# Optimization experiments

Measured on AMD Instinct MI355X. Metric: run time of the kernel, lower is better.

The kernel has to match this reference:

```python
import jax, jax.numpy as jnp
import numpy as np

EMB = 64
B, L = 4096, 200
N_USERS, N_ITEMS, N_RATE, N_RANK, N_SPEC = 100000, 100000, 6, 128, 64
EPS = 1e-10


def _mlp2(x, w1, b1, w2, b2):
    # Linear -> ReLU -> Linear  (torch MLP: in -> in//2 -> out)
    return jax.nn.relu(x @ w1 + b1) @ w2 + b2


def setup_inputs() -> dict:
    key = jax.random.key(0)
    ks = jax.random.split(key, 32)
    s = 0.02
    d = {}
    d["user_tab"] = jax.random.normal(ks[0], (N_USERS, EMB), jnp.float32) * s
    d["item_tab"] = jax.random.normal(ks[1], (N_ITEMS, EMB), jnp.float32) * s
    d["rating_tab"] = jax.random.normal(ks[2], (N_RATE, EMB), jnp.float32) * s
    d["ranking_tab"] = jax.random.normal(ks[3], (N_RANK, EMB), jnp.float32) * s
    d["species_tab"] = jax.random.normal(ks[4], (N_SPEC, EMB), jnp.float32) * s
    # g_u: MLP(2E -> E): Linear(2E, E), ReLU, Linear(E, E)
    d["gu_w1"] = jax.random.normal(ks[5], (2 * EMB, EMB), jnp.float32) * s
    d["gu_b1"] = jnp.zeros((EMB,), jnp.float32)
    d["gu_w2"] = jax.random.normal(ks[6], (EMB, EMB), jnp.float32) * s
    d["gu_b2"] = jnp.zeros((EMB,), jnp.float32)
    # item_users_attn: MLP(2E -> 1): Linear(2E, E), ReLU, Linear(E, 1)
    d["at_w1"] = jax.random.normal(ks[7], (2 * EMB, EMB), jnp.float32) * s
    d["at_b1"] = jnp.zeros((EMB,), jnp.float32)
    d["at_w2"] = jax.random.normal(ks[8], (EMB, 1), jnp.float32) * s
    d["at_b2"] = jnp.zeros((1,), jnp.float32)
    # aggr_users: Linear(E, E) + ReLU
    d["ag_w"] = jax.random.normal(ks[9], (EMB, EMB), jnp.float32) * s
    d["ag_b"] = jnp.zeros((EMB,), jnp.float32)
    # final mlp: Linear(2E,E) ReLU Linear(E,E) ReLU Linear(E,E) ReLU
    d["m_w1"] = jax.random.normal(ks[10], (2 * EMB, EMB), jnp.float32) * s
    d["m_b1"] = jnp.zeros((EMB,), jnp.float32)
    d["m_w2"] = jax.random.normal(ks[11], (EMB, EMB), jnp.float32) * s
    d["m_b2"] = jnp.zeros((EMB,), jnp.float32)
    d["m_w3"] = jax.random.normal(ks[12], (EMB, EMB), jnp.float32) * s
    d["m_b3"] = jnp.zeros((EMB,), jnp.float32)
    # int inputs
    d["iids"] = jax.random.randint(ks[13], (B,), 0, N_ITEMS, jnp.int64 if jax.config.jax_enable_x64 else jnp.int32)
    d["i_user_pad"] = jnp.stack([
        jax.random.randint(ks[14], (B, L), 0, N_USERS),
        jax.random.randint(ks[15], (B, L), 0, N_RATE)], axis=-1)
    d["i_userk_pad"] = jnp.stack([
        jax.random.randint(ks[16], (B, L), 0, N_USERS),
        jax.random.randint(ks[17], (B, L), 0, N_RANK)], axis=-1)
    d["i_user_species_pad"] = jnp.stack([
        jax.random.randint(ks[18], (B, L), 0, N_USERS),
        jax.random.randint(ks[19], (B, L), 0, N_SPEC)], axis=-1)
    return d


def _attn_aggregate(f_jt, q_j, mask, at_w1, at_b1, at_w2, at_b2, ag_w, ag_b):
    # masked exp-softmax attention over neighbor axis + weighted sum + aggregator
    mu = _mlp2(jnp.concatenate([f_jt, q_j], axis=-1), at_w1, at_b1, at_w2, at_b2)[..., 0]  # [B, L]
    mu = jnp.exp(mu) * mask
    mu = mu / (jnp.sum(mu, axis=1, keepdims=True) + EPS)
    z = jnp.einsum('bl,bld->bd', mu, f_jt)
    return jax.nn.relu(z @ ag_w + ag_b)


def reference(user_tab, item_tab, rating_tab, ranking_tab, species_tab,
              gu_w1, gu_b1, gu_w2, gu_b2,
              at_w1, at_b1, at_w2, at_b2,
              ag_w, ag_b,
              m_w1, m_b1, m_w2, m_b2, m_w3, m_b3,
              iids, i_user_pad, i_userk_pad, i_user_species_pad):
    p_t = user_tab[i_user_pad[:, :, 0]]            # [B, L, E]
    i_user_er = rating_tab[i_user_pad[:, :, 1]]    # [B, L, E]
    mask = (i_user_pad[:, :, 0] > 0).astype(p_t.dtype)  # [B, L]
    q_j = jnp.broadcast_to(item_tab[iids][:, None, :], p_t.shape)  # [B, L, E]

    # branch 1: species-modulated
    spec = species_tab[i_user_species_pad[:, :, 1]]
    f1 = _mlp2(jnp.concatenate([p_t, spec], axis=-1), gu_w1, gu_b1, gu_w2, gu_b2) * i_user_er
    z_j1 = _attn_aggregate(f1, q_j, mask, at_w1, at_b1, at_w2, at_b2, ag_w, ag_b)

    # branch 2: ranking-modulated, double g_u
    nk = ranking_tab[i_userk_pad[:, :, 1]]
    f2 = _mlp2(jnp.concatenate([p_t, i_user_er], axis=-1), gu_w1, gu_b1, gu_w2, gu_b2) * nk
    f2 = _mlp2(jnp.concatenate([p_t, f2], axis=-1), gu_w1, gu_b1, gu_w2, gu_b2)
    z_j2 = _attn_aggregate(f2, q_j, mask, at_w1, at_b1, at_w2, at_b2, ag_w, ag_b)

    # final 3-layer MLP with ReLU after each layer
    h = jax.nn.relu(jnp.concatenate([z_j1, z_j2], axis=1) @ m_w1 + m_b1)
    h = jax.nn.relu(h @ m_w2 + m_b2)
    h = jax.nn.relu(h @ m_w3 + m_b3)
    return h
```

## Files before the change

### kernel.cpp

```cpp
#include <hip/hip_runtime.h>

#define EPSV 1e-10f
#define XS 68

typedef __attribute__((__ext_vector_type__(8))) short  bhalf8;
typedef __attribute__((__ext_vector_type__(4))) float  f4;
typedef __attribute__((__ext_vector_type__(4))) unsigned u4;

#define MFMA(a,b,c) __builtin_amdgcn_mfma_f32_16x16x32_bf16(a,b,c,0,0,0)

__device__ __forceinline__ bhalf8 ldb16(const unsigned* p) {
    u4 v = *(const u4*)p;
    return __builtin_bit_cast(bhalf8, v);
}

__device__ __forceinline__ void split8(f4 a, f4 b, bhalf8& h, bhalf8& l) {
    float ff[8] = {a[0],a[1],a[2],a[3],b[0],b[1],b[2],b[3]};
    unsigned uh[8]; float fl[8];
#pragma unroll
    for (int i = 0; i < 8; ++i) {
        unsigned bits = __float_as_uint(ff[i]);
        uh[i] = bits & 0xFFFF0000u;
        fl[i] = ff[i] - __uint_as_float(uh[i]);
    }
    u4 hv = { (uh[0]>>16)|uh[1], (uh[2]>>16)|uh[3], (uh[4]>>16)|uh[5], (uh[6]>>16)|uh[7] };
    u4 lv = { (__float_as_uint(fl[0])>>16)|(__float_as_uint(fl[1])&0xFFFF0000u),
              (__float_as_uint(fl[2])>>16)|(__float_as_uint(fl[3])&0xFFFF0000u),
              (__float_as_uint(fl[4])>>16)|(__float_as_uint(fl[5])&0xFFFF0000u),
              (__float_as_uint(fl[6])>>16)|(__float_as_uint(fl[7])&0xFFFF0000u) };
    h = __builtin_bit_cast(bhalf8, hv);
    l = __builtin_bit_cast(bhalf8, lv);
}

__device__ __forceinline__ void gemm6(f4 acc[4],
                                      bhalf8 ah0, bhalf8 al0, bhalf8 ah1, bhalf8 al1,
                                      const unsigned* Bhi, const unsigned* Blo, int lane) {
    bhalf8 bh0 = ldb16(Bhi + (0 * 64 + lane) * 4);
    bhalf8 bh1 = ldb16(Bhi + (4 * 64 + lane) * 4);
    bhalf8 bl0 = ldb16(Blo + (0 * 64 + lane) * 4);
    bhalf8 bl1 = ldb16(Blo + (4 * 64 + lane) * 4);
#pragma unroll
    for (int t = 0; t < 4; ++t) {
        bhalf8 nh0, nh1, nl0, nl1;
        if (t < 3) {
            nh0 = ldb16(Bhi + ((t + 1) * 64 + lane) * 4);
            nh1 = ldb16(Bhi + ((t + 5) * 64 + lane) * 4);
            nl0 = ldb16(Blo + ((t + 1) * 64 + lane) * 4);
            nl1 = ldb16(Blo + ((t + 5) * 64 + lane) * 4);
        }
        acc[t] = MFMA(ah0, bh0, acc[t]);
        acc[t] = MFMA(ah1, bh1, acc[t]);
        acc[t] = MFMA(al0, bh0, acc[t]);
        acc[t] = MFMA(al1, bh1, acc[t]);
        acc[t] = MFMA(ah0, bl0, acc[t]);
        acc[t] = MFMA(ah1, bl1, acc[t]);
        __builtin_amdgcn_sched_barrier(0);
        if (t < 3) { bh0 = nh0; bh1 = nh1; bl0 = nl0; bl1 = nl1; }
    }
}

__device__ __forceinline__ void ldA(const float* Xb, int arow, int lane,
                                    bhalf8& h0, bhalf8& l0, bhalf8& h1, bhalf8& l1) {
    const float* p = Xb + arow * XS + ((lane >> 4) * 8);
    split8(*(const f4*)p,        *(const f4*)(p + 4),  h0, l0);
    split8(*(const f4*)(p + 32), *(const f4*)(p + 36), h1, l1);
}

__global__ void prep_tables_k(const float* __restrict__ species_tab,
                              const float* __restrict__ rating_tab,
                              const float* __restrict__ gu_w1,
                              float* __restrict__ spec2, float* __restrict__ rate2) {
    int tid = blockIdx.x * blockDim.x + threadIdx.x;
    if (tid >= 70 * 64) return;
    int row = tid >> 6, e = tid & 63;
    const float* src = (row < 64) ? (species_tab + row * 64) : (rating_tab + (row - 64) * 64);
    float acc = 0.f;
#pragma unroll 8
    for (int k = 0; k < 64; ++k) acc += src[k] * gu_w1[(64 + k) * 64 + e];
    if (row < 64) spec2[row * 64 + e] = acc;
    else          rate2[(row - 64) * 64 + e] = acc;
}

__global__ void prep_qat_k(const float* __restrict__ item_tab, const int* __restrict__ iids,
                           const float* __restrict__ at_w1, const float* __restrict__ at_b1,
                           float* __restrict__ qat, int B) {
    int tid = blockIdx.x * blockDim.x + threadIdx.x;
    if (tid >= B * 64) return;
    int b = tid >> 6, e = tid & 63;
    const float* q = item_tab + (long)iids[b] * 64;
    float acc = at_b1[e];
#pragma unroll 8
    for (int k = 0; k < 64; ++k) acc += q[k] * at_w1[(64 + k) * 64 + e];
    qat[tid] = acc;
}

__global__ void pack_frags_k(const float* __restrict__ gu_w2, const float* __restrict__ at_w1,
                             const float* __restrict__ gu_w1, unsigned* __restrict__ dst) {
    int tid = blockIdx.x * blockDim.x + threadIdx.x;
    if (tid >= 4 * 8 * 64) return;
    int lane = tid & 63, fi = (tid >> 6) & 7, mat = tid >> 9;
    const float* M = (mat == 0) ? gu_w2 : (mat == 1) ? at_w1 : (mat == 2) ? gu_w1 : gu_w1 + 64 * 64;
    int s = fi >> 2, t = fi & 3;
    int n = t * 16 + (lane & 15);
    int kb = s * 32 + (lane >> 4) * 8;
    unsigned hi[4], lo[4];
#pragma unroll
    for (int d = 0; d < 4; ++d) {
        float f0 = M[(kb + 2 * d) * 64 + n], f1 = M[(kb + 2 * d + 1) * 64 + n];
        unsigned b0 = __float_as_uint(f0), b1 = __float_as_uint(f1);
        unsigned h0 = b0 & 0xFFFF0000u, h1 = b1 & 0xFFFF0000u;
        hi[d] = (b0 >> 16) | h1;
        float l0 = f0 - __uint_as_float(h0), l1 = f1 - __uint_as_float(h1);
        lo[d] = (__float_as_uint(l0) >> 16) | (__float_as_uint(l1) & 0xFFFF0000u);
    }
    unsigned* hp = dst + (size_t)mat * 4096 + (size_t)(fi * 64 + lane) * 4;
    unsigned* lp = hp + 2048;
    *(u4*)hp = u4{hi[0], hi[1], hi[2], hi[3]};
    *(u4*)lp = u4{lo[0], lo[1], lo[2], lo[3]};
}

__global__ __launch_bounds__(256, 2) void item_main_k(
    const float* __restrict__ user_tab, const float* __restrict__ rating_tab,
    const float* __restrict__ ranking_tab,
    const float* __restrict__ gu_b1, const float* __restrict__ gu_b2,
    const float* __restrict__ at_w2, const float* __restrict__ at_b2,
    const float* __restrict__ ag_w, const float* __restrict__ ag_b,
    const float* __restrict__ m_w1, const float* __restrict__ m_b1,
    const float* __restrict__ m_w2, const float* __restrict__ m_b2,
    const float* __restrict__ m_w3, const float* __restrict__ m_b3,
    const int* __restrict__ i_user_pad, const int* __restrict__ i_userk_pad,
    const int* __restrict__ i_user_species_pad,
    const unsigned* __restrict__ frg,
    const float* __restrict__ spec2, const float* __restrict__ rate2,
    const float* __restrict__ qat,
    float* __restrict__ out, int L)
{
    __shared__ unsigned WL[8192];
    __shared__ float X[64 * XS];
    __shared__ float U[64 * XS];
    __shared__ int   uidxb[256], ridb[256], sidb[256], kidb[256];
    __shared__ float ZW[4][2][64];
    __shared__ float DW[4][2];
    __shared__ float fin[320];

    const int b    = blockIdx.x;
    const int tid  = threadIdx.x;
    const int lane = tid & 63;
    const int wv   = __builtin_amdgcn_readfirstlane(tid >> 6);

    {
        const u4* src = (const u4*)frg;
        u4* dst = (u4*)WL;
#pragma unroll
        for (int i = 0; i < 8; ++i) dst[tid + i * 256] = src[tid + i * 256];
    }
    {
        int l = tid;
        int u = 0, rr = 0, ss = 0, kk = 0;
        if (l < L) {
            long base = (long)b * L + l;
            u  = i_user_pad[base * 2 + 0];
            rr = i_user_pad[base * 2 + 1];
            ss = i_user_species_pad[base * 2 + 1];
            kk = i_userk_pad[base * 2 + 1];
        }
        uidxb[l] = u; ridb[l] = rr; sidb[l] = ss; kidb[l] = kk;
    }
    __syncthreads();

    float qatv[4], aw2v[4], b1v[4], b2v[4];
#pragma unroll
    for (int t = 0; t < 4; ++t) {
        int col = t * 16 + (lane & 15);
        qatv[t] = qat[b * 64 + col];
        aw2v[t] = at_w2[col];
        b1v[t]  = gu_b1[col];
        b2v[t]  = gu_b2[col];
    }
    const float ab2 = at_b2[0];

    const f4 z4 = {0.f, 0.f, 0.f, 0.f};
    f4 zac0 = z4, zac1 = z4;
    float den0 = 0.f, den1 = 0.f;

    const int arow  = wv * 16 + (lane & 15);
    const int drow0 = wv * 16 + (lane >> 4) * 4;
    const int lcol  = lane & 15;

    const int nch = (L + 63) >> 6;
    for (int chunk = 0; chunk < nch; ++chunk) {
        const int cbase = chunk * 64;

        int rid4[4], sid4[4], kid4[4];
#pragma unroll
        for (int r = 0; r < 4; ++r) {
            int gt = cbase + drow0 + r;
            rid4[r] = ridb[gt]; sid4[r] = sidb[gt]; kid4[r] = kidb[gt];
        }

        bhalf8 ah0, al0, ah1, al1;

        {
            const float* pr = user_tab + (size_t)uidxb[cbase + arow] * 64 + ((lane >> 4) * 8);
            split8(*(const f4*)pr,        *(const f4*)(pr + 4),  ah0, al0);
            split8(*(const f4*)(pr + 32), *(const f4*)(pr + 36), ah1, al1);
        }
        {
            f4 u1[4] = {z4, z4, z4, z4};
            gemm6(u1, ah0, al0, ah1, al1, frg + 8192, frg + 8192 + 2048, lane);
#pragma unroll
            for (int t = 0; t < 4; ++t) {
                int col = t * 16 + lcol;
#pragma unroll
                for (int r = 0; r < 4; ++r) {
                    float up = u1[t][r] + b1v[t];
                    U[(drow0 + r) * XS + col] = up;
                    float v = up + spec2[sid4[r] * 64 + col];
                    X[(drow0 + r) * XS + col] = v > 0.f ? v : 0.f;
                }
            }
        }

        ldA(X, arow, lane, ah0, al0, ah1, al1);
        {
            f4 fk[4] = {z4, z4, z4, z4};
            gemm6(fk, ah0, al0, ah1, al1, WL, WL + 2048, lane);
#pragma unroll
            for (int t = 0; t < 4; ++t) {
                int col = t * 16 + lcol;
#pragma unroll
                for (int r = 0; r < 4; ++r)
                    X[(drow0 + r) * XS + col] =
                        (fk[t][r] + b2v[t]) * rating_tab[rid4[r] * 64 + col];
            }
        }

        ldA(X, arow, lane, ah0, al0, ah1, al1);
        {
            f4 t1[4] = {z4, z4, z4, z4};
            gemm6(t1, ah0, al0, ah1, al1, WL + 4096, WL + 4096 + 2048, lane);
            float pd[4];
#pragma unroll
            for (int r = 0; r < 4; ++r) {
                float s = 0.f;
#pragma unroll
                for (int t = 0; t < 4; ++t) {
                    float v = t1[t][r] + qatv[t];
                    v = v > 0.f ? v : 0.f;
                    s += v * aw2v[t];
                }
                pd[r] = s;
            }
#pragma unroll
            for (int m = 1; m < 16; m <<= 1)
#pragma unroll
                for (int r = 0; r < 4; ++r) pd[r] += __shfl_xor(pd[r], m, 64);
            float w[4];
#pragma unroll
            for (int r = 0; r < 4; ++r)
                w[r] = (uidxb[cbase + drow0 + r] > 0) ? __expf(pd[r] + ab2) : 0.f;
            float ds = w[0] + w[1] + w[2] + w[3];
            ds += __shfl_xor(ds, 16, 64); ds += __shfl_xor(ds, 32, 64);
            den0 += ds;
#pragma unroll
            for (int t = 0; t < 4; ++t) {
                int col = t * 16 + lcol;
                float s = w[0] * X[(drow0 + 0) * XS + col] + w[1] * X[(drow0 + 1) * XS + col]
                        + w[2] * X[(drow0 + 2) * XS + col] + w[3] * X[(drow0 + 3) * XS + col];
                s += __shfl_xor(s, 16, 64); s += __shfl_xor(s, 32, 64);
                zac0[t] += s;
            }
        }

#pragma unroll
        for (int t = 0; t < 4; ++t) {
            int col = t * 16 + lcol;
#pragma unroll
            for (int r = 0; r < 4; ++r) {
                float v = U[(drow0 + r) * XS + col] + rate2[rid4[r] * 64 + col];
                X[(drow0 + r) * XS + col] = v > 0.f ? v : 0.f;
            }
        }
        ldA(X, arow, lane, ah0, al0, ah1, al1);
        {
            f4 f2[4] = {z4, z4, z4, z4};
            gemm6(f2, ah0, al0, ah1, al1, WL, WL + 2048, lane);
#pragma unroll
            for (int t = 0; t < 4; ++t) {
                int col = t * 16 + lcol;
#pragma unroll
                for (int r = 0; r < 4; ++r)
                    X[(drow0 + r) * XS + col] =
                        (f2[t][r] + b2v[t]) * ranking_tab[kid4[r] * 64 + col];
            }
        }

        ldA(X, arow, lane, ah0, al0, ah1, al1);
        {
            f4 fb1[4] = {z4, z4, z4, z4};
            gemm6(fb1, ah0, al0, ah1, al1, frg + 12288, frg + 12288 + 2048, lane);
#pragma unroll
            for (int t = 0; t < 4; ++t) {
                int col = t * 16 + lcol;
#pragma unroll
                for (int r = 0; r < 4; ++r) {
                    float v = fb1[t][r] + U[(drow0 + r) * XS + col];
                    X[(drow0 + r) * XS + col] = v > 0.f ? v : 0.f;
                }
            }
        }
        ldA(X, arow, lane, ah0, al0, ah1, al1);
        {
            f4 f2[4] = {z4, z4, z4, z4};
            gemm6(f2, ah0, al0, ah1, al1, WL, WL + 2048, lane);
#pragma unroll
            for (int t = 0; t < 4; ++t) {
                int col = t * 16 + lcol;
#pragma unroll
                for (int r = 0; r < 4; ++r)
                    X[(drow0 + r) * XS + col] = f2[t][r] + b2v[t];
            }
        }

        ldA(X, arow, lane, ah0, al0, ah1, al1);
        {
            f4 t2[4] = {z4, z4, z4, z4};
            gemm6(t2, ah0, al0, ah1, al1, WL + 4096, WL + 4096 + 2048, lane);
            float pd[4];
#pragma unroll
            for (int r = 0; r < 4; ++r) {
                float s = 0.f;
#pragma unroll
                for (int t = 0; t < 4; ++t) {
                    float v = t2[t][r] + qatv[t];
                    v = v > 0.f ? v : 0.f;
                    s += v * aw2v[t];
                }
                pd[r] = s;
            }
#pragma unroll
            for (int m = 1; m < 16; m <<= 1)
#pragma unroll
                for (int r = 0; r < 4; ++r) pd[r] += __shfl_xor(pd[r], m, 64);
            float w[4];
#pragma unroll
            for (int r = 0; r < 4; ++r)
                w[r] = (uidxb[cbase + drow0 + r] > 0) ? __expf(pd[r] + ab2) : 0.f;
            float ds = w[0] + w[1] + w[2] + w[3];
            ds += __shfl_xor(ds, 16, 64); ds += __shfl_xor(ds, 32, 64);
            den1 += ds;
#pragma unroll
            for (int t = 0; t < 4; ++t) {
                int col = t * 16 + lcol;
                float s = w[0] * X[(drow0 + 0) * XS + col] + w[1] * X[(drow0 + 1) * XS + col]
                        + w[2] * X[(drow0 + 2) * XS + col] + w[3] * X[(drow0 + 3) * XS + col];
                s += __shfl_xor(s, 16, 64); s += __shfl_xor(s, 32, 64);
                zac1[t] += s;
            }
        }
    }

    if (lane < 16) {
#pragma unroll
        for (int t = 0; t < 4; ++t) {
            ZW[wv][0][t * 16 + lane] = zac0[t];
            ZW[wv][1][t * 16 + lane] = zac1[t];
        }
    }
    if (lane == 0) { DW[wv][0] = den0; DW[wv][1] = den1; }
    __syncthreads();

    float* znorm = fin;
    float* hcat  = fin + 128;
    float* hv    = fin + 256;
    if (tid < 128) {
        int att = tid >> 6, e = tid & 63;
        float z  = ZW[0][att][e] + ZW[1][att][e] + ZW[2][att][e] + ZW[3][att][e];
        float dn = DW[0][att] + DW[1][att] + DW[2][att] + DW[3][att] + EPSV;
        znorm[tid] = z / dn;
    }
    __syncthreads();
    if (tid < 128) {
        int e = tid & 63, half = tid >> 6;
        float a = ag_b[e];
        const float* zn = znorm + half * 64;
#pragma unroll 4
        for (int k = 0; k < 64; ++k) a += zn[k] * ag_w[k * 64 + e];
        hcat[tid] = a > 0.f ? a : 0.f;
    }
    __syncthreads();
    if (tid < 64) {
        float a = m_b1[tid];
#pragma unroll 4
        for (int k = 0; k < 128; ++k) a += hcat[k] * m_w1[k * 64 + tid];
        hv[tid] = a > 0.f ? a : 0.f;
    }
    __syncthreads();
    if (tid < 64) {
        float a = m_b2[tid];
#pragma unroll 4
        for (int k = 0; k < 64; ++k) a += hv[k] * m_w2[k * 64 + tid];
        znorm[tid] = a > 0.f ? a : 0.f;
    }
    __syncthreads();
    if (tid < 64) {
        float a = m_b3[tid];
#pragma unroll 4
        for (int k = 0; k < 64; ++k) a += znorm[k] * m_w3[k * 64 + tid];
        out[(long)b * 64 + tid] = a > 0.f ? a : 0.f;
    }
}

extern "C" void kernel_launch(void* const* d_in, const int* in_sizes, int n_in,
                              void* d_out, int out_size, void* d_ws, size_t ws_size,
                              hipStream_t stream) {
    const float* user_tab    = (const float*)d_in[0];
    const float* item_tab    = (const float*)d_in[1];
    const float* rating_tab  = (const float*)d_in[2];
    const float* ranking_tab = (const float*)d_in[3];
    const float* species_tab = (const float*)d_in[4];
    const float* gu_w1 = (const float*)d_in[5];
    const float* gu_b1 = (const float*)d_in[6];
    const float* gu_w2 = (const float*)d_in[7];
    const float* gu_b2 = (const float*)d_in[8];
    const float* at_w1 = (const float*)d_in[9];
    const float* at_b1 = (const float*)d_in[10];
    const float* at_w2 = (const float*)d_in[11];
    const float* at_b2 = (const float*)d_in[12];
    const float* ag_w  = (const float*)d_in[13];
    const float* ag_b  = (const float*)d_in[14];
    const float* m_w1  = (const float*)d_in[15];
    const float* m_b1  = (const float*)d_in[16];
    const float* m_w2  = (const float*)d_in[17];
    const float* m_b2  = (const float*)d_in[18];
    const float* m_w3  = (const float*)d_in[19];
    const float* m_b3  = (const float*)d_in[20];
    const int* iids               = (const int*)d_in[21];
    const int* i_user_pad         = (const int*)d_in[22];
    const int* i_userk_pad        = (const int*)d_in[23];
    const int* i_user_species_pad = (const int*)d_in[24];

    const int B = in_sizes[21];
    const int L = in_sizes[22] / (B * 2);

    unsigned* frg  = (unsigned*)d_ws;
    float* spec2 = (float*)d_ws + 16384;
    float* rate2 = spec2 + 4096;
    float* qat   = rate2 + 384;

    prep_tables_k<<<(70 * 64 + 255) / 256, 256, 0, stream>>>(species_tab, rating_tab, gu_w1,
                                                             spec2, rate2);
    prep_qat_k<<<(B * 64 + 255) / 256, 256, 0, stream>>>(item_tab, iids, at_w1, at_b1, qat, B);
    pack_frags_k<<<8, 256, 0, stream>>>(gu_w2, at_w1, gu_w1, frg);
    item_main_k<<<B, 256, 0, stream>>>(user_tab, rating_tab, ranking_tab,
                                       gu_b1, gu_b2, at_w2, at_b2, ag_w, ag_b,
                                       m_w1, m_b1, m_w2, m_b2, m_w3, m_b3,
                                       i_user_pad, i_userk_pad, i_user_species_pad,
                                       frg, spec2, rate2, qat, (float*)d_out, L);
}
```

Baseline: 350.0 us.

## Switch split-bf16 MFMA to scaled fp16 MFMA and precompute user projection table

The three-pass split-bf16 GEMMs (six MFMAs per tile) are replaced with single-pass fp16 MFMAs. Operands are pre-scaled by powers of two so they stay in fp16 range, and the results are rescaled afterwards. The first-layer projection of every user embedding through gu_w1 is precomputed into a full 100k-row table by a new kernel, so the main kernel gathers these rows instead of running a GEMM per chunk. This removes much of the per-row MFMA work, at the cost of fp16 rounding error and an extra pass that reads and writes the whole user table every call.

```diff
diff --git a/kernel.cpp b/kernel.cpp
--- a/kernel.cpp
+++ b/kernel.cpp
@@ -2,68 +2,54 @@
 
 #define EPSV 1e-10f
 #define XS 68
-
-typedef __attribute__((__ext_vector_type__(8))) short  bhalf8;
+#define SA 16384.0f
+#define SB 1024.0f
+#define C10 9.765625e-4f
+#define C24 5.9604644775390625e-8f
+#define C14 6.103515625e-5f
+
+typedef __attribute__((__ext_vector_type__(8))) _Float16 half8;
+typedef __attribute__((__ext_vector_type__(2))) __fp16   fp16x2;
 typedef __attribute__((__ext_vector_type__(4))) float  f4;
 typedef __attribute__((__ext_vector_type__(4))) unsigned u4;
 
-#define MFMA(a,b,c) __builtin_amdgcn_mfma_f32_16x16x32_bf16(a,b,c,0,0,0)
-
-__device__ __forceinline__ bhalf8 ldb16(const unsigned* p) {
+#define MF16(a,b,c) __builtin_amdgcn_mfma_f32_16x16x32_f16(a,b,c,0,0,0)
+
+__device__ __forceinline__ half8 ldh(const unsigned* p) {
     u4 v = *(const u4*)p;
-    return __builtin_bit_cast(bhalf8, v);
-}
-
-__device__ __forceinline__ void split8(f4 a, f4 b, bhalf8& h, bhalf8& l) {
-    float ff[8] = {a[0],a[1],a[2],a[3],b[0],b[1],b[2],b[3]};
-    unsigned uh[8]; float fl[8];
-#pragma unroll
-    for (int i = 0; i < 8; ++i) {
-        unsigned bits = __float_as_uint(ff[i]);
-        uh[i] = bits & 0xFFFF0000u;
-        fl[i] = ff[i] - __uint_as_float(uh[i]);
-    }
-    u4 hv = { (uh[0]>>16)|uh[1], (uh[2]>>16)|uh[3], (uh[4]>>16)|uh[5], (uh[6]>>16)|uh[7] };
-    u4 lv = { (__float_as_uint(fl[0])>>16)|(__float_as_uint(fl[1])&0xFFFF0000u),
-              (__float_as_uint(fl[2])>>16)|(__float_as_uint(fl[3])&0xFFFF0000u),
-              (__float_as_uint(fl[4])>>16)|(__float_as_uint(fl[5])&0xFFFF0000u),
-              (__float_as_uint(fl[6])>>16)|(__float_as_uint(fl[7])&0xFFFF0000u) };
-    h = __builtin_bit_cast(bhalf8, hv);
-    l = __builtin_bit_cast(bhalf8, lv);
-}
-
-__device__ __forceinline__ void gemm6(f4 acc[4],
-                                      bhalf8 ah0, bhalf8 al0, bhalf8 ah1, bhalf8 al1,
-                                      const unsigned* Bhi, const unsigned* Blo, int lane) {
-    bhalf8 bh0 = ldb16(Bhi + (0 * 64 + lane) * 4);
-    bhalf8 bh1 = ldb16(Bhi + (4 * 64 + lane) * 4);
-    bhalf8 bl0 = ldb16(Blo + (0 * 64 + lane) * 4);
-    bhalf8 bl1 = ldb16(Blo + (4 * 64 + lane) * 4);
-#pragma unroll
-    for (int t = 0; t < 4; ++t) {
-        bhalf8 nh0, nh1, nl0, nl1;
-        if (t < 3) {
-            nh0 = ldb16(Bhi + ((t + 1) * 64 + lane) * 4);
-            nh1 = ldb16(Bhi + ((t + 5) * 64 + lane) * 4);
-            nl0 = ldb16(Blo + ((t + 1) * 64 + lane) * 4);
-            nl1 = ldb16(Blo + ((t + 5) * 64 + lane) * 4);
-        }
-        acc[t] = MFMA(ah0, bh0, acc[t]);
-        acc[t] = MFMA(ah1, bh1, acc[t]);
-        acc[t] = MFMA(al0, bh0, acc[t]);
-        acc[t] = MFMA(al1, bh1, acc[t]);
-        acc[t] = MFMA(ah0, bl0, acc[t]);
-        acc[t] = MFMA(ah1, bl1, acc[t]);
-        __builtin_amdgcn_sched_barrier(0);
-        if (t < 3) { bh0 = nh0; bh1 = nh1; bl0 = nl0; bl1 = nl1; }
-    }
-}
-
-__device__ __forceinline__ void ldA(const float* Xb, int arow, int lane,
-                                    bhalf8& h0, bhalf8& l0, bhalf8& h1, bhalf8& l1) {
+    return __builtin_bit_cast(half8, v);
+}
+
+__device__ __forceinline__ half8 cvt8(f4 a, f4 b) {
+    fp16x2 p0 = __builtin_amdgcn_cvt_pkrtz(a[0], a[1]);
+    fp16x2 p1 = __builtin_amdgcn_cvt_pkrtz(a[2], a[3]);
+    fp16x2 p2 = __builtin_amdgcn_cvt_pkrtz(b[0], b[1]);
+    fp16x2 p3 = __builtin_amdgcn_cvt_pkrtz(b[2], b[3]);
+    u4 r = { __builtin_bit_cast(unsigned, p0), __builtin_bit_cast(unsigned, p1),
+             __builtin_bit_cast(unsigned, p2), __builtin_bit_cast(unsigned, p3) };
+    return __builtin_bit_cast(half8, r);
+}
+
+__device__ __forceinline__ void ldAf(const float* Xb, int arow, int lane,
+                                     half8& a0, half8& a1) {
     const float* p = Xb + arow * XS + ((lane >> 4) * 8);
-    split8(*(const f4*)p,        *(const f4*)(p + 4),  h0, l0);
-    split8(*(const f4*)(p + 32), *(const f4*)(p + 36), h1, l1);
+    a0 = cvt8(*(const f4*)p,        *(const f4*)(p + 4));
+    a1 = cvt8(*(const f4*)(p + 32), *(const f4*)(p + 36));
+}
+
+__device__ __forceinline__ void gemmf(f4 acc[4], half8 a0, half8 a1,
+                                      const unsigned* B, int lane) {
+    half8 b0[4], b1[4];
+#pragma unroll
+    for (int t = 0; t < 4; ++t) b0[t] = ldh(B + (t * 64 + lane) * 4);
+#pragma unroll
+    for (int t = 0; t < 4; ++t) b1[t] = ldh(B + ((4 + t) * 64 + lane) * 4);
+#pragma unroll
+    for (int t = 0; t < 4; ++t) acc[t] = MF16(a0, b0[t], acc[t]);
+    __builtin_amdgcn_sched_barrier(0);
+#pragma unroll
+    for (int t = 0; t < 4; ++t) acc[t] = MF16(a1, b1[t], acc[t]);
+    __builtin_amdgcn_sched_barrier(0);
 }
 
 __global__ void prep_tables_k(const float* __restrict__ species_tab,
@@ -77,8 +63,8 @@
     float acc = 0.f;
 #pragma unroll 8
     for (int k = 0; k < 64; ++k) acc += src[k] * gu_w1[(64 + k) * 64 + e];
-    if (row < 64) spec2[row * 64 + e] = acc;
-    else          rate2[(row - 64) * 64 + e] = acc;
+    if (row < 64) spec2[row * 64 + e] = acc * SA;
+    else          rate2[(row - 64) * 64 + e] = acc * SA;
 }
 
 __global__ void prep_qat_k(const float* __restrict__ item_tab, const int* __restrict__ iids,
@@ -94,35 +80,43 @@
     qat[tid] = acc;
 }
 
+__global__ void u1tab_k(const float* __restrict__ user_tab, const float* __restrict__ gu_w1,
+                        const float* __restrict__ gu_b1, float* __restrict__ u1tab, int NU) {
+    int tid = blockIdx.x * blockDim.x + threadIdx.x;
+    if (tid >= NU * 64) return;
+    int u = tid >> 6, e = tid & 63;
+    const float* p = user_tab + (size_t)u * 64;
+    float acc = gu_b1[e];
+#pragma unroll 8
+    for (int k = 0; k < 64; ++k) acc += p[k] * gu_w1[k * 64 + e];
+    u1tab[tid] = acc * SA;
+}
+
 __global__ void pack_frags_k(const float* __restrict__ gu_w2, const float* __restrict__ at_w1,
                              const float* __restrict__ gu_w1, unsigned* __restrict__ dst) {
     int tid = blockIdx.x * blockDim.x + threadIdx.x;
-    if (tid >= 4 * 8 * 64) return;
+    if (tid >= 3 * 8 * 64) return;
     int lane = tid & 63, fi = (tid >> 6) & 7, mat = tid >> 9;
-    const float* M = (mat == 0) ? gu_w2 : (mat == 1) ? at_w1 : (mat == 2) ? gu_w1 : gu_w1 + 64 * 64;
+    const float* M = (mat == 0) ? gu_w2 : (mat == 1) ? at_w1 : gu_w1 + 64 * 64;
     int s = fi >> 2, t = fi & 3;
-    int n = t * 16 + (lane & 15);
+    int n  = t * 16 + (lane & 15);
     int kb = s * 32 + (lane >> 4) * 8;
-    unsigned hi[4], lo[4];
+    unsigned dw[4];
 #pragma unroll
     for (int d = 0; d < 4; ++d) {
-        float f0 = M[(kb + 2 * d) * 64 + n], f1 = M[(kb + 2 * d + 1) * 64 + n];
-        unsigned b0 = __float_as_uint(f0), b1 = __float_as_uint(f1);
-        unsigned h0 = b0 & 0xFFFF0000u, h1 = b1 & 0xFFFF0000u;
-        hi[d] = (b0 >> 16) | h1;
-        float l0 = f0 - __uint_as_float(h0), l1 = f1 - __uint_as_float(h1);
-        lo[d] = (__float_as_uint(l0) >> 16) | (__float_as_uint(l1) & 0xFFFF0000u);
-    }
-    unsigned* hp = dst + (size_t)mat * 4096 + (size_t)(fi * 64 + lane) * 4;
-    unsigned* lp = hp + 2048;
-    *(u4*)hp = u4{hi[0], hi[1], hi[2], hi[3]};
-    *(u4*)lp = u4{lo[0], lo[1], lo[2], lo[3]};
+        _Float16 h0 = (_Float16)(M[(kb + 2 * d) * 64 + n] * SB);
+        _Float16 h1 = (_Float16)(M[(kb + 2 * d + 1) * 64 + n] * SB);
+        unsigned lo = (unsigned)__builtin_bit_cast(unsigned short, h0);
+        unsigned hi = (unsigned)__builtin_bit_cast(unsigned short, h1);
+        dw[d] = lo | (hi << 16);
+    }
+    *(u4*)(dst + (size_t)mat * 2048 + (size_t)(fi * 64 + lane) * 4) = u4{dw[0], dw[1], dw[2], dw[3]};
 }
 
 __global__ __launch_bounds__(256, 2) void item_main_k(
-    const float* __restrict__ user_tab, const float* __restrict__ rating_tab,
+    const float* __restrict__ u1tab, const float* __restrict__ rating_tab,
     const float* __restrict__ ranking_tab,
-    const float* __restrict__ gu_b1, const float* __restrict__ gu_b2,
+    const float* __restrict__ gu_b2,
     const float* __restrict__ at_w2, const float* __restrict__ at_b2,
     const float* __restrict__ ag_w, const float* __restrict__ ag_b,
     const float* __restrict__ m_w1, const float* __restrict__ m_b1,
@@ -135,7 +129,7 @@
     const float* __restrict__ qat,
     float* __restrict__ out, int L)
 {
-    __shared__ unsigned WL[8192];
+    __shared__ unsigned WL[6144];
     __shared__ float X[64 * XS];
     __shared__ float U[64 * XS];
     __shared__ int   uidxb[256], ridb[256], sidb[256], kidb[256];
@@ -152,7 +146,7 @@
         const u4* src = (const u4*)frg;
         u4* dst = (u4*)WL;
 #pragma unroll
-        for (int i = 0; i < 8; ++i) dst[tid + i * 256] = src[tid + i * 256];
+        for (int i = 0; i < 6; ++i) dst[tid + i * 256] = src[tid + i * 256];
     }
     {
         int l = tid;
@@ -168,14 +162,13 @@
     }
     __syncthreads();
 
-    float qatv[4], aw2v[4], b1v[4], b2v[4];
+    float qatv[4], aw2v[4], b2v[4];
 #pragma unroll
     for (int t = 0; t < 4; ++t) {
         int col = t * 16 + (lane & 15);
         qatv[t] = qat[b * 64 + col];
         aw2v[t] = at_w2[col];
-        b1v[t]  = gu_b1[col];
-        b2v[t]  = gu_b2[col];
+        b2v[t]  = gu_b2[col] * SA;
     }
     const float ab2 = at_b2[0];
 
@@ -186,66 +179,68 @@
     const int arow  = wv * 16 + (lane & 15);
     const int drow0 = wv * 16 + (lane >> 4) * 4;
     const int lcol  = lane & 15;
+    const int koff  = (lane >> 4) * 8;
 
     const int nch = (L + 63) >> 6;
     for (int chunk = 0; chunk < nch; ++chunk) {
         const int cbase = chunk * 64;
 
-        int rid4[4], sid4[4], kid4[4];
+        int rid4[4], kid4[4];
 #pragma unroll
         for (int r = 0; r < 4; ++r) {
             int gt = cbase + drow0 + r;
-            rid4[r] = ridb[gt]; sid4[r] = sidb[gt]; kid4[r] = kidb[gt];
-        }
-
-        bhalf8 ah0, al0, ah1, al1;
-
-        {
-            const float* pr = user_tab + (size_t)uidxb[cbase + arow] * 64 + ((lane >> 4) * 8);
-            split8(*(const f4*)pr,        *(const f4*)(pr + 4),  ah0, al0);
-            split8(*(const f4*)(pr + 32), *(const f4*)(pr + 36), ah1, al1);
-        }
-        {
-            f4 u1[4] = {z4, z4, z4, z4};
-            gemm6(u1, ah0, al0, ah1, al1, frg + 8192, frg + 8192 + 2048, lane);
-#pragma unroll
-            for (int t = 0; t < 4; ++t) {
-                int col = t * 16 + lcol;
-#pragma unroll
-                for (int r = 0; r < 4; ++r) {
-                    float up = u1[t][r] + b1v[t];
-                    U[(drow0 + r) * XS + col] = up;
-                    float v = up + spec2[sid4[r] * 64 + col];
-                    X[(drow0 + r) * XS + col] = v > 0.f ? v : 0.f;
-                }
-            }
-        }
-
-        ldA(X, arow, lane, ah0, al0, ah1, al1);
+            rid4[r] = ridb[gt]; kid4[r] = kidb[gt];
+        }
+
+        half8 a0, a1;
+
+        {
+            const int rowid = cbase + arow;
+            const float* pr = u1tab + (size_t)uidxb[rowid] * 64 + koff;
+            const float* sp = spec2 + sidb[rowid] * 64 + koff;
+            f4 ua = *(const f4*)pr,        ub = *(const f4*)(pr + 4);
+            f4 uc = *(const f4*)(pr + 32), ud = *(const f4*)(pr + 36);
+            f4 sa_ = *(const f4*)sp,        sb_ = *(const f4*)(sp + 4);
+            f4 sc_ = *(const f4*)(sp + 32), sd_ = *(const f4*)(sp + 36);
+            float* up = U + arow * XS + koff;
+            float* xp = X + arow * XS + koff;
+            *(f4*)up = ua; *(f4*)(up + 4) = ub; *(f4*)(up + 32) = uc; *(f4*)(up + 36) = ud;
+            f4 r0, r1, r2, r3;
+#pragma unroll
+            for (int j = 0; j < 4; ++j) {
+                r0[j] = fmaxf(ua[j] + sa_[j], 0.f);
+                r1[j] = fmaxf(ub[j] + sb_[j], 0.f);
+                r2[j] = fmaxf(uc[j] + sc_[j], 0.f);
+                r3[j] = fmaxf(ud[j] + sd_[j], 0.f);
+            }
+            *(f4*)xp = r0; *(f4*)(xp + 4) = r1; *(f4*)(xp + 32) = r2; *(f4*)(xp + 36) = r3;
+        }
+
+        ldAf(X, arow, lane, a0, a1);
         {
             f4 fk[4] = {z4, z4, z4, z4};
-            gemm6(fk, ah0, al0, ah1, al1, WL, WL + 2048, lane);
+            gemmf(fk, a0, a1, WL, lane);
 #pragma unroll
             for (int t = 0; t < 4; ++t) {
                 int col = t * 16 + lcol;
 #pragma unroll
                 for (int r = 0; r < 4; ++r)
                     X[(drow0 + r) * XS + col] =
-                        (fk[t][r] + b2v[t]) * rating_tab[rid4[r] * 64 + col];
-            }
-        }
-
-        ldA(X, arow, lane, ah0, al0, ah1, al1);
+                        fmaf(fk[t][r], C10, b2v[t]) * rating_tab[rid4[r] * 64 + col];
+            }
+        }
+
+        ldAf(X, arow, lane, a0, a1);
         {
             f4 t1[4] = {z4, z4, z4, z4};
-            gemm6(t1, ah0, al0, ah1, al1, WL + 4096, WL + 4096 + 2048, lane);
+            gemmf(t1, a0, a1, WL + 2048, lane);
             float pd[4];
 #pragma unroll
             for (int r = 0; r < 4; ++r) {
                 float s = 0.f;
 #pragma unroll
                 for (int t = 0; t < 4; ++t) {
-                    float v = t1[t][r] + qatv[t];
+                    float v = fmaf(t1[t][r], C24, qatv[t]);
                     v = v > 0.f ? v : 0.f;
                     s += v * aw2v[t];
                 }
@@ -272,67 +267,77 @@
             }
         }
 
-#pragma unroll
-        for (int t = 0; t < 4; ++t) {
-            int col = t * 16 + lcol;
-#pragma unroll
-            for (int r = 0; r < 4; ++r) {
-                float v = U[(drow0 + r) * XS + col] + rate2[rid4[r] * 64 + col];
-                X[(drow0 + r) * XS + col] = v > 0.f ? v : 0.f;
-            }
-        }
-        ldA(X, arow, lane, ah0, al0, ah1, al1);
+        {
+            const int rowid = cbase + arow;
+            const float* rp = rate2 + ridb[rowid] * 64 + koff;
+            const float* up = U + arow * XS + koff;
+            float* xp = X + arow * XS + koff;
+            f4 ra = *(const f4*)rp,        rb = *(const f4*)(rp + 4);
+            f4 rc = *(const f4*)(rp + 32), rd = *(const f4*)(rp + 36);
+            f4 ua = *(const f4*)up,        ub = *(const f4*)(up + 4);
+            f4 uc = *(const f4*)(up + 32), ud = *(const f4*)(up + 36);
+            f4 r0, r1, r2, r3;
+#pragma unroll
+            for (int j = 0; j < 4; ++j) {
+                r0[j] = fmaxf(ua[j] + ra[j], 0.f);
+                r1[j] = fmaxf(ub[j] + rb[j], 0.f);
+                r2[j] = fmaxf(uc[j] + rc[j], 0.f);
+                r3[j] = fmaxf(ud[j] + rd[j], 0.f);
+            }
+            *(f4*)xp = r0; *(f4*)(xp + 4) = r1; *(f4*)(xp + 32) = r2; *(f4*)(xp + 36) = r3;
+        }
+        ldAf(X, arow, lane, a0, a1);
         {
             f4 f2[4] = {z4, z4, z4, z4};
-            gemm6(f2, ah0, al0, ah1, al1, WL, WL + 2048, lane);
+            gemmf(f2, a0, a1, WL, lane);
 #pragma unroll
             for (int t = 0; t < 4; ++t) {
                 int col = t * 16 + lcol;
 #pragma unroll
                 for (int r = 0; r < 4; ++r)
                     X[(drow0 + r) * XS + col] =
-                        (f2[t][r] + b2v[t]) * ranking_tab[kid4[r] * 64 + col];
-            }
-        }
-
-        ldA(X, arow, lane, ah0, al0, ah1, al1);
+                        fmaf(f2[t][r], C10, b2v[t]) * ranking_tab[kid4[r] * 64 + col];
+            }
+        }
+
+        ldAf(X, arow, lane, a0, a1);
         {
             f4 fb1[4] = {z4, z4, z4, z4};
-            gemm6(fb1, ah0, al0, ah1, al1, frg + 12288, frg + 12288 + 2048, lane);
+            gemmf(fb1, a0, a1, WL + 4096, lane);
 #pragma unroll
             for (int t = 0; t < 4; ++t) {
                 int col = t * 16 + lcol;
 #pragma unroll
                 for (int r = 0; r < 4; ++r) {
-                    float v = fb1[t][r] + U[(drow0 + r) * XS + col];
+                    float v = fmaf(fb1[t][r], C10, U[(drow0 + r) * XS + col]);
                     X[(drow0 + r) * XS + col] = v > 0.f ? v : 0.f;
                 }
             }
         }
-        ldA(X, arow, lane, ah0, al0, ah1, al1);
+        ldAf(X, arow, lane, a0, a1);
         {
             f4 f2[4] = {z4, z4, z4, z4};
-            gemm6(f2, ah0, al0, ah1, al1, WL, WL + 2048, lane);
+            gemmf(f2, a0, a1, WL, lane);
 #pragma unroll
             for (int t = 0; t < 4; ++t) {
                 int col = t * 16 + lcol;
 #pragma unroll
                 for (int r = 0; r < 4; ++r)
-                    X[(drow0 + r) * XS + col] = f2[t][r] + b2v[t];
-            }
-        }
-
-        ldA(X, arow, lane, ah0, al0, ah1, al1);
+                    X[(drow0 + r) * XS + col] = fmaf(f2[t][r], C10, b2v[t]);
+            }
+        }
+
+        ldAf(X, arow, lane, a0, a1);
         {
             f4 t2[4] = {z4, z4, z4, z4};
-            gemm6(t2, ah0, al0, ah1, al1, WL + 4096, WL + 4096 + 2048, lane);
+            gemmf(t2, a0, a1, WL + 2048, lane);
             float pd[4];
 #pragma unroll
             for (int r = 0; r < 4; ++r) {
                 float s = 0.f;
 #pragma unroll
                 for (int t = 0; t < 4; ++t) {
-                    float v = t2[t][r] + qatv[t];
+                    float v = fmaf(t2[t][r], C24, qatv[t]);
                     v = v > 0.f ? v : 0.f;
                     s += v * aw2v[t];
                 }
@@ -363,8 +368,8 @@
     if (lane < 16) {
 #pragma unroll
         for (int t = 0; t < 4; ++t) {
-            ZW[wv][0][t * 16 + lane] = zac0[t];
-            ZW[wv][1][t * 16 + lane] = zac1[t];
+            ZW[wv][0][t * 16 + lane] = zac0[t] * C14;
+            ZW[wv][1][t * 16 + lane] = zac1[t] * C14;
         }
     }
     if (lane == 0) { DW[wv][0] = den0; DW[wv][1] = den1; }
@@ -440,20 +445,23 @@
     const int* i_userk_pad        = (const int*)d_in[23];
     const int* i_user_species_pad = (const int*)d_in[24];
 
-    const int B = in_sizes[21];
-    const int L = in_sizes[22] / (B * 2);
-
-    unsigned* frg  = (unsigned*)d_ws;
-    float* spec2 = (float*)d_ws + 16384;
+    const int B  = in_sizes[21];
+    const int L  = in_sizes[22] / (B * 2);
+    const int NU = in_sizes[0] / 64;
+
+    unsigned* frg = (unsigned*)d_ws;
+    float* spec2 = (float*)d_ws + 6144;
     float* rate2 = spec2 + 4096;
     float* qat   = rate2 + 384;
+    float* u1tab = qat + (size_t)B * 64;
 
     prep_tables_k<<<(70 * 64 + 255) / 256, 256, 0, stream>>>(species_tab, rating_tab, gu_w1,
                                                              spec2, rate2);
     prep_qat_k<<<(B * 64 + 255) / 256, 256, 0, stream>>>(item_tab, iids, at_w1, at_b1, qat, B);
-    pack_frags_k<<<8, 256, 0, stream>>>(gu_w2, at_w1, gu_w1, frg);
-    item_main_k<<<B, 256, 0, stream>>>(user_tab, rating_tab, ranking_tab,
-                                       gu_b1, gu_b2, at_w2, at_b2, ag_w, ag_b,
+    u1tab_k<<<(NU * 64 + 255) / 256, 256, 0, stream>>>(user_tab, gu_w1, gu_b1, u1tab, NU);
+    pack_frags_k<<<6, 256, 0, stream>>>(gu_w2, at_w1, gu_w1, frg);
+    item_main_k<<<B, 256, 0, stream>>>(u1tab, rating_tab, ranking_tab,
+                                       gu_b2, at_w2, at_b2, ag_w, ag_b,
                                        m_w1, m_b1, m_w2, m_b2, m_w3, m_b3,
                                        i_user_pad, i_userk_pad, i_user_species_pad,
                                        frg, spec2, rate2, qat, (float*)d_out, L);
```

After: 396.7 us. +13.3%, slower.
